# Optimization experiments

Measured on AMD Instinct MI355X. Metric: run time of the kernel, lower is better.

The kernel has to match this reference:

```python
import jax, jax.numpy as jnp
import numpy as np


def setup_inputs() -> dict:
    key = jax.random.key(0)
    k1, k2, k3, k4 = jax.random.split(key, 4)
    B, C_in, KH, KW, C_out = 256, 512, 7, 7, 1000
    inputR = jax.random.normal(k1, (B, C_in, KH, KW), dtype=jnp.float32)
    inputSPD = jax.random.normal(k2, (B, C_in, C_in), dtype=jnp.float32)
    fan_in = C_in * KH * KW
    weight = jax.random.normal(k3, (C_out, C_in, KH, KW), dtype=jnp.float32) / np.sqrt(fan_in)
    bias = jax.random.normal(k4, (C_out,), dtype=jnp.float32) / np.sqrt(fan_in)
    return {"inputR": inputR, "inputSPD": inputSPD, "weight": weight, "bias": bias}


def reference(inputR, inputSPD, weight, bias):
    # Conv2d with kernel == spatial size and padding 0 == fully connected layer.
    # outputR: (N, C_out)
    outputR = jnp.einsum('nchw,ochw->no', inputR, weight) + bias

    # top-2 channel selection per sample (indices only; values unused)
    _, top2_idx = jax.lax.top_k(outputR, 2)  # (N, 2)

    # weight is detached for the SPD path in the original module
    w_spd = jax.lax.stop_gradient(weight)[top2_idx]  # (N, 2, C_in, KH, KW)

    # outputSPD[n,k,m] = sum_{c,d,h,w} SPD[n,c,d] * W2[n,k,d,h,w] * W2[n,m,c,h,w]
    # (equivalent to the original's two batched matmuls + sum over (h, w))
    outputSPD = jnp.einsum('ncd,nkdhw,nmchw->nkm', inputSPD, w_spd, w_spd)  # (N, 2, 2)
    return outputR, outputSPD
```

## Files before the change

kernel.cpp:

```cpp
#include <hip/hip_runtime.h>

#define KD 25088
#define N_DIM 1000
#define ZS 28

typedef __attribute__((ext_vector_type(8))) short bf16x8;
typedef __attribute__((ext_vector_type(4))) float f32x4;

__device__ inline unsigned pack2(float a, float b) {
  unsigned r;
  asm("v_cvt_pk_bf16_f32 %0, %1, %2" : "=v"(r) : "v"(a), "v"(b));
  return r;
}
__device__ inline unsigned short f2bf(float x) {
  unsigned r;
  asm("v_cvt_pk_bf16_f32 %0, %1, %1" : "=v"(r) : "v"(x));
  return (unsigned short)r;
}
__device__ inline float bf2f(unsigned short u) {
  union { unsigned u; float f; } v; v.u = ((unsigned)u) << 16; return v.f;
}

__global__ __launch_bounds__(256) void init_bias_k(
    const float* __restrict__ bias, float* __restrict__ outR) {
  const int id = blockIdx.x * 256 + threadIdx.x;
  if (id < 256 * N_DIM) outR[id] = bias[id % N_DIM];
}

template<int ATOMIC>
__global__ __launch_bounds__(256) void rgemm_k(
    const float* __restrict__ A, const float* __restrict__ W,
    float* __restrict__ D) {
  __shared__ unsigned short As[2][128 * 32];
  __shared__ unsigned short Bs[2][128 * 32];
  const int t = threadIdx.x;
  const int id  = blockIdx.x;
  const int mz  = (id & 7) * 7 + ((id >> 3) >> 3);
  const int n0  = ((id >> 3) & 7) * 128;
  const int m0  = (mz / ZS) * 128;
  const int z   = mz % ZS;
  const int lane = t & 63, w = t >> 6;
  const int cw = (w >> 1) * 64, jw = (w & 1) * 64;
  const int r16 = lane & 15, quad = lane >> 4;
  const int srow = t >> 2;
  const int sc8  = (t & 3) << 3;
  const bool doj3 = (n0 + jw + 48) < N_DIM;

  float a_pre[16], b_pre[16];

  f32x4 acc[4][4];
#pragma unroll
  for (int i = 0; i < 4; ++i)
#pragma unroll
    for (int j = 0; j < 4; ++j) {
      acc[i][j][0] = 0.f; acc[i][j][1] = 0.f;
      acc[i][j][2] = 0.f; acc[i][j][3] = 0.f;
    }

#define RG_LOAD(s_)                                                         \
  {                                                                         \
    const int kbase = ((z) * ZS + (s_)) * 32;                               \
    _Pragma("unroll")                                                       \
    for (int h = 0; h < 2; ++h) {                                           \
      const int row = h * 64 + srow;                                        \
      const float* pa = A + (size_t)(m0 + row) * KD + kbase + sc8;          \
      *(float4*)&a_pre[h * 8 + 0] = *(const float4*)pa;                     \
      *(float4*)&a_pre[h * 8 + 4] = *(const float4*)(pa + 4);               \
      const int wr = n0 + row;                                              \
      if (wr < N_DIM) {                                                     \
        const float* pw = W + (size_t)wr * KD + kbase + sc8;                \
        *(float4*)&b_pre[h * 8 + 0] = *(const float4*)pw;                   \
        *(float4*)&b_pre[h * 8 + 4] = *(const float4*)(pw + 4);             \
      } else {                                                              \
        _Pragma("unroll")                                                   \
        for (int q = 0; q < 8; ++q) b_pre[h * 8 + q] = 0.f;                 \
      }                                                                     \
    }                                                                       \
  }

#define RG_WRITE(p_)                                                        \
  {                                                                         \
    _Pragma("unroll")                                                       \
    for (int h = 0; h < 2; ++h) {                                           \
      const int row = h * 64 + srow;                                        \
      uint4 ua, ub;                                                         \
      ua.x = pack2(a_pre[h*8+0], a_pre[h*8+1]);                             \
      ua.y = pack2(a_pre[h*8+2], a_pre[h*8+3]);                             \
      ua.z = pack2(a_pre[h*8+4], a_pre[h*8+5]);                             \
      ua.w = pack2(a_pre[h*8+6], a_pre[h*8+7]);                             \
      ub.x = pack2(b_pre[h*8+0], b_pre[h*8+1]);                             \
      ub.y = pack2(b_pre[h*8+2], b_pre[h*8+3]);                             \
      ub.z = pack2(b_pre[h*8+4], b_pre[h*8+5]);                             \
      ub.w = pack2(b_pre[h*8+6], b_pre[h*8+7]);                             \
      *(uint4*)&As[p_][row * 32 + sc8] = ua;                                \
      *(uint4*)&Bs[p_][row * 32 + sc8] = ub;                                \
    }                                                                       \
  }

  RG_LOAD(0); RG_WRITE(0); __syncthreads();
  int p = 0;
  for (int s = 0; s < ZS; ++s) {
    if (s + 1 < ZS) RG_LOAD(s + 1);
    bf16x8 af[4], bq[4];
#pragma unroll
    for (int i = 0; i < 4; ++i) {
      af[i] = *(const bf16x8*)&As[p][(cw + i * 16 + r16) * 32 + quad * 8];
      if (i < 3 || doj3)
        bq[i] = *(const bf16x8*)&Bs[p][(jw + i * 16 + r16) * 32 + quad * 8];
    }
#pragma unroll
    for (int i = 0; i < 4; ++i)
#pragma unroll
      for (int j = 0; j < 4; ++j)
        if (j < 3 || doj3)
          acc[i][j] = __builtin_amdgcn_mfma_f32_16x16x32_bf16(af[i], bq[j], acc[i][j], 0, 0, 0);
    if (s + 1 < ZS) RG_WRITE(p ^ 1);
    __syncthreads();
    p ^= 1;
  }

#pragma unroll
  for (int j = 0; j < 4; ++j) {
    const int n = n0 + jw + j * 16 + r16;
    if (n < N_DIM) {
#pragma unroll
      for (int i = 0; i < 4; ++i)
#pragma unroll
        for (int r = 0; r < 4; ++r) {
          const int m = m0 + cw + i * 16 + quad * 4 + r;
          if (ATOMIC)
            atomicAdd(&D[(size_t)m * N_DIM + n], acc[i][j][r]);
          else
            D[((size_t)z * 256 + m) * N_DIM + n] = acc[i][j][r];
        }
    }
  }
#undef RG_LOAD
#undef RG_WRITE
}

template<int FROMPART>
__global__ __launch_bounds__(64) void top8_k(
    const float* __restrict__ src, const float* __restrict__ bias,
    float* __restrict__ outR, int* __restrict__ top2,
    int* __restrict__ candIdx, int* __restrict__ flags,
    float* __restrict__ outSPD) {
  const int n = blockIdx.x;
  const int lane = threadIdx.x;
  float v[16];
  if (FROMPART) {
#pragma unroll
    for (int r = 0; r < 16; ++r) {
      const int o = lane + r * 64;
      v[r] = (o < N_DIM) ? bias[o] : -3.0e38f;
    }
    for (int z = 0; z < ZS; ++z) {
      const float* pz = src + ((size_t)z * 256 + n) * N_DIM;
#pragma unroll
      for (int r = 0; r < 16; ++r) {
        const int o = lane + r * 64;
        if (o < N_DIM) v[r] += pz[o];
      }
    }
#pragma unroll
    for (int r = 0; r < 16; ++r) {
      const int o = lane + r * 64;
      if (o < N_DIM) outR[(size_t)n * N_DIM + o] = v[r];
    }
  } else {
#pragma unroll
    for (int r = 0; r < 16; ++r) {
      const int o = lane + r * 64;
      v[r] = (o < N_DIM) ? src[(size_t)n * N_DIM + o] : -3.0e38f;
    }
  }
  float cv[8]; int ci[8];
#pragma unroll
  for (int rr = 0; rr < 8; ++rr) {
    float bv = -3.0e38f; int bi = 0x3fffffff;
#pragma unroll
    for (int r = 0; r < 16; ++r) {
      const int o = lane + r * 64;
      if (v[r] > bv || (v[r] == bv && o < bi)) { bv = v[r]; bi = o; }
    }
#pragma unroll
    for (int off = 32; off >= 1; off >>= 1) {
      const float ov = __shfl_xor(bv, off, 64);
      const int   oi = __shfl_xor(bi, off, 64);
      if (ov > bv || (ov == bv && oi < bi)) { bv = ov; bi = oi; }
    }
    cv[rr] = bv; ci[rr] = bi;
#pragma unroll
    for (int r = 0; r < 16; ++r)
      if (lane + r * 64 == bi) v[r] = -3.0e38f;
  }
  if (lane == 0) {
    const bool safe = (cv[0] - cv[1] >= 0.025f) &&
                      (cv[1] - cv[2] >= 0.025f) &&
                      (cv[1] - cv[7] >= 0.05f);
    flags[n] = safe ? 0 : 1;
    top2[2 * n]     = ci[0];
    top2[2 * n + 1] = ci[1];
#pragma unroll
    for (int r = 0; r < 8; ++r) candIdx[n * 8 + r] = ci[r];
    outSPD[4 * n + 0] = 0.f; outSPD[4 * n + 1] = 0.f;
    outSPD[4 * n + 2] = 0.f; outSPD[4 * n + 3] = 0.f;
  }
}

__global__ __launch_bounds__(256) void rdot_k(
    const float* __restrict__ A, const float* __restrict__ W,
    const float* __restrict__ bias, const int* __restrict__ candIdx,
    const int* __restrict__ flags, float* __restrict__ vals) {
  const int n = blockIdx.x;
  if (!flags[n]) return;
  const int c = blockIdx.y;
  const int idx = candIdx[n * 8 + c];
  const float4* a4 = (const float4*)(A + (size_t)n * KD);
  const float4* w4 = (const float4*)(W + (size_t)idx * KD);
  float s = 0.f;
  for (int i = threadIdx.x; i < KD / 4; i += 256) {
    const float4 av = a4[i];
    const float4 wv = w4[i];
    s += av.x * wv.x + av.y * wv.y + av.z * wv.z + av.w * wv.w;
  }
#pragma unroll
  for (int off = 32; off >= 1; off >>= 1) s += __shfl_xor(s, off, 64);
  __shared__ float red[4];
  const int lane = threadIdx.x & 63, w = threadIdx.x >> 6;
  if (lane == 0) red[w] = s;
  __syncthreads();
  if (threadIdx.x == 0)
    vals[n * 8 + c] = red[0] + red[1] + red[2] + red[3] + bias[idx];
}

__global__ __launch_bounds__(64) void select_k(
    const float* __restrict__ vals, const int* __restrict__ candIdx,
    const int* __restrict__ flags, int* __restrict__ top2) {
  const int n = blockIdx.x;
  if (threadIdx.x != 0 || !flags[n]) return;
  int b0 = -1; float v0 = -3.0e38f; int i0 = 0x3fffffff;
  for (int c = 0; c < 8; ++c) {
    const int idx = candIdx[n * 8 + c];
    const float vv = vals[n * 8 + c];
    if (vv > v0 || (vv == v0 && idx < i0)) { v0 = vv; i0 = idx; b0 = c; }
  }
  float v1 = -3.0e38f; int i1 = 0x3fffffff;
  for (int c = 0; c < 8; ++c) {
    if (c == b0) continue;
    const int idx = candIdx[n * 8 + c];
    const float vv = vals[n * 8 + c];
    if (vv > v1 || (vv == v1 && idx < i1)) { v1 = vv; i1 = idx; }
  }
  top2[2 * n]     = i0;
  top2[2 * n + 1] = i1;
}

__global__ __launch_bounds__(256) void packsel_k(
    const float* __restrict__ W, const int* __restrict__ candIdx,
    const int* __restrict__ flags, const float* __restrict__ vals,
    unsigned short* __restrict__ Wp) {
  __shared__ unsigned short tile[49 * 130];
  __shared__ int sel_s;
  const int n = blockIdx.x;
  const int which = blockIdx.y;
  const int t = threadIdx.x;
  if (t == 0) {
    int ia, ib;
    if (!flags[n]) {
      ia = candIdx[n * 8];
      ib = candIdx[n * 8 + 1];
    } else {
      int b0 = -1; float v0 = -3.0e38f; int i0 = 0x3fffffff;
      for (int c = 0; c < 8; ++c) {
        const int idx = candIdx[n * 8 + c];
        const float vv = vals[n * 8 + c];
        if (vv > v0 || (vv == v0 && idx < i0)) { v0 = vv; i0 = idx; b0 = c; }
      }
      float v1 = -3.0e38f; int i1 = 0x3fffffff;
      for (int c = 0; c < 8; ++c) {
        if (c == b0) continue;
        const int idx = candIdx[n * 8 + c];
        const float vv = vals[n * 8 + c];
        if (vv > v1 || (vv == v1 && idx < i1)) { v1 = vv; i1 = idx; }
      }
      ia = i0; ib = i1;
    }
    sel_s = which ? ib : ia;
  }
  unsigned short* dstn = Wp + (size_t)n * 65536;
  {
    const int r0 = 98 + which * 15;
    for (int u = t; u < 15 * 128; u += 256) {
      const int rr = u >> 7;
      const int cc = (u & 127) << 1;
      *(unsigned*)(dstn + (size_t)(r0 + rr) * 512 + cc) = 0u;
    }
  }
  __syncthreads();
  const int sel = sel_s;
  const float4* src4 = (const float4*)(W + (size_t)sel * KD);
  for (int chunk = 0; chunk < 4; ++chunk) {
    const float4* s4 = src4 + chunk * 1568;
    for (int u4 = t; u4 < 1568; u4 += 256) {
      const float4 fv = s4[u4];
      const float vv[4] = {fv.x, fv.y, fv.z, fv.w};
      const int i0 = u4 * 4;
#pragma unroll
      for (int e = 0; e < 4; ++e) {
        const int idx = i0 + e;
        const int c = idx / 49;
        const int hw = idx - c * 49;
        tile[hw * 130 + c] = f2bf(vv[e]);
      }
    }
    __syncthreads();
    const int cp = t & 63, hwb = t >> 6;
    unsigned short* wbase = dstn + (size_t)which * 49 * 512 + chunk * 128 + 2 * cp;
#pragma unroll
    for (int it = 0; it < 13; ++it) {
      const int hw = hwb + it * 4;
      if (hw < 49) {
        const unsigned val = *(const unsigned*)&tile[hw * 130 + 2 * cp];
        *(unsigned*)(wbase + (size_t)hw * 512) = val;
      }
    }
    __syncthreads();
  }
}

__global__ __launch_bounds__(256) void spd_k(
    const float* __restrict__ S, const unsigned short* __restrict__ Wp,
    float* __restrict__ outSPD) {
  __shared__ unsigned short As[2][128 * 32];
  __shared__ unsigned short Bs[2][128 * 32];
  __shared__ float red[4];
  const int t = threadIdx.x;
  const int id = blockIdx.x;
  const int n  = (id & 7) * 32 + ((id >> 3) >> 2);
  const int c0 = ((id >> 3) & 3) * 128;
  const float* Sn = S + (size_t)n * 512 * 512;
  const unsigned short* Wpn = Wp + (size_t)n * 65536;
  const int lane = t & 63, w = t >> 6;
  const int cw = (w >> 1) * 64, jw = (w & 1) * 64;
  const int r16 = lane & 15, quad = lane >> 4;
  const int srow = t >> 2;
  const int sc8  = (t & 3) << 3;
  const bool doj3 = (jw == 0);

  if (t < 4) red[t] = 0.f;

  float a_pre[16];
  uint4 b_pre[2];

  f32x4 acc[4][4];
#pragma unroll
  for (int i = 0; i < 4; ++i)
#pragma unroll
    for (int j = 0; j < 4; ++j) {
      acc[i][j][0] = 0.f; acc[i][j][1] = 0.f;
      acc[i][j][2] = 0.f; acc[i][j][3] = 0.f;
    }

#define SP_LOAD(s_)                                                         \
  {                                                                         \
    const int d0 = (s_) * 32;                                               \
    _Pragma("unroll")                                                       \
    for (int h = 0; h < 2; ++h) {                                           \
      const int row = h * 64 + srow;                                        \
      const float* pa = Sn + (size_t)(c0 + row) * 512 + d0 + sc8;           \
      *(float4*)&a_pre[h * 8 + 0] = *(const float4*)pa;                     \
      *(float4*)&a_pre[h * 8 + 4] = *(const float4*)(pa + 4);               \
      b_pre[h] = *(const uint4*)(Wpn + (size_t)row * 512 + d0 + sc8);       \
    }                                                                       \
  }

#define SP_WRITE(p_)                                                        \
  {                                                                         \
    _Pragma("unroll")                                                       \
    for (int h = 0; h < 2; ++h) {                                           \
      const int row = h * 64 + srow;                                        \
      uint4 ua;                                                             \
      ua.x = pack2(a_pre[h*8+0], a_pre[h*8+1]);                             \
      ua.y = pack2(a_pre[h*8+2], a_pre[h*8+3]);                             \
      ua.z = pack2(a_pre[h*8+4], a_pre[h*8+5]);                             \
      ua.w = pack2(a_pre[h*8+6], a_pre[h*8+7]);                             \
      *(uint4*)&As[p_][row * 32 + sc8] = ua;                                \
      *(uint4*)&Bs[p_][row * 32 + sc8] = b_pre[h];                          \
    }                                                                       \
  }

  SP_LOAD(0); SP_WRITE(0); __syncthreads();
  int p = 0;
  for (int s = 0; s < 16; ++s) {
    if (s + 1 < 16) SP_LOAD(s + 1);
    bf16x8 af[4], bq[4];
#pragma unroll
    for (int i = 0; i < 4; ++i) {
      af[i] = *(const bf16x8*)&As[p][(cw + i * 16 + r16) * 32 + quad * 8];
      if (i < 3 || doj3)
        bq[i] = *(const bf16x8*)&Bs[p][(jw + i * 16 + r16) * 32 + quad * 8];
    }
#pragma unroll
    for (int i = 0; i < 4; ++i)
#pragma unroll
      for (int j = 0; j < 4; ++j)
        if (j < 3 || doj3)
          acc[i][j] = __builtin_amdgcn_mfma_f32_16x16x32_bf16(af[i], bq[j], acc[i][j], 0, 0, 0);
    if (s + 1 < 16) SP_WRITE(p ^ 1);
    __syncthreads();
    p ^= 1;
  }
#undef SP_LOAD
#undef SP_WRITE

  float p00 = 0.f, p01 = 0.f, p10 = 0.f, p11 = 0.f;
#pragma unroll
  for (int j = 0; j < 4; ++j) {
    const int jj = jw + j * 16 + r16;
    if (jj < 98) {
      const int kk = (jj >= 49);
      const int hw = jj - 49 * kk;
      const unsigned short* wa = Wpn + (size_t)hw * 512;
      const unsigned short* wb = Wpn + (size_t)(49 + hw) * 512;
#pragma unroll
      for (int i = 0; i < 4; ++i) {
#pragma unroll
        for (int r = 0; r < 4; ++r) {
          const int c = c0 + cw + i * 16 + quad * 4 + r;
          const float u   = acc[i][j][r];
          const float wav = bf2f(wa[c]);
          const float wbv = bf2f(wb[c]);
          if (kk == 0) { p00 = fmaf(u, wav, p00); p01 = fmaf(u, wbv, p01); }
          else         { p10 = fmaf(u, wav, p10); p11 = fmaf(u, wbv, p11); }
        }
      }
    }
  }

  atomicAdd(&red[0], p00);
  atomicAdd(&red[1], p01);
  atomicAdd(&red[2], p10);
  atomicAdd(&red[3], p11);
  __syncthreads();
  if (t < 4) atomicAdd(&outSPD[n * 4 + t], red[t]);
}

__global__ __launch_bounds__(256) void spd_fb_k(
    const float* __restrict__ S, const float* __restrict__ W,
    const int* __restrict__ top2, float* __restrict__ outSPD) {
  __shared__ unsigned short As[128 * 40];
  __shared__ unsigned short Bs[128 * 40];
  __shared__ float red[4];
  const int t = threadIdx.x;
  const int n  = blockIdx.x >> 2;
  const int c0 = (blockIdx.x & 3) * 128;
  const int ia = top2[2 * n];
  const int ib = top2[2 * n + 1];
  const float* Sn = S + (size_t)n * 512 * 512;
  const int lane = t & 63, w = t >> 6;
  const int cw = (w >> 1) * 64, jw = (w & 1) * 64;
  const int r16 = lane & 15, quad = lane >> 4;
  if (t < 4) red[t] = 0.f;
  f32x4 acc[4][4];
#pragma unroll
  for (int i = 0; i < 4; ++i)
#pragma unroll
    for (int j = 0; j < 4; ++j) {
      acc[i][j][0] = 0.f; acc[i][j][1] = 0.f;
      acc[i][j][2] = 0.f; acc[i][j][3] = 0.f;
    }
  const int bj  = t & 127;
  const int bh  = t >> 7;
  const int bkk = (bj >= 49);
  const int bhw = bj - 49 * bkk;
  const bool bvalid = (bj < 98);
  const float* brow = W + (size_t)(bkk ? ib : ia) * KD + bhw;
  for (int d0 = 0; d0 < 512; d0 += 32) {
#pragma unroll
    for (int h = 0; h < 4; ++h) {
      const int idx = h * 256 + t;
      const int row = idx >> 3;
      const int c4  = (idx & 7) << 2;
      float4 av = *(const float4*)(Sn + (size_t)(c0 + row) * 512 + d0 + c4);
      uint2 pa;
      pa.x = pack2(av.x, av.y);
      pa.y = pack2(av.z, av.w);
      *(uint2*)&As[row * 40 + c4] = pa;
    }
#pragma unroll
    for (int dd2 = 0; dd2 < 16; dd2 += 2) {
      const int dd = bh * 16 + dd2;
      const float x0 = bvalid ? brow[(size_t)(d0 + dd) * 49] : 0.f;
      const float x1 = bvalid ? brow[(size_t)(d0 + dd + 1) * 49] : 0.f;
      *(unsigned*)&Bs[bj * 40 + dd] = pack2(x0, x1);
    }
    __syncthreads();
    bf16x8 af[4], bq[4];
#pragma unroll
    for (int i = 0; i < 4; ++i) {
      af[i] = *(const bf16x8*)&As[(cw + i * 16 + r16) * 40 + quad * 8];
      bq[i] = *(const bf16x8*)&Bs[(jw + i * 16 + r16) * 40 + quad * 8];
    }
#pragma unroll
    for (int i = 0; i < 4; ++i)
#pragma unroll
      for (int j = 0; j < 4; ++j)
        acc[i][j] = __builtin_amdgcn_mfma_f32_16x16x32_bf16(af[i], bq[j], acc[i][j], 0, 0, 0);
    __syncthreads();
  }
  float p00 = 0.f, p01 = 0.f, p10 = 0.f, p11 = 0.f;
  const float* Wa = W + (size_t)ia * KD;
  const float* Wb = W + (size_t)ib * KD;
#pragma unroll
  for (int j = 0; j < 4; ++j) {
    const int jj = jw + j * 16 + r16;
    if (jj < 98) {
      const int kk = (jj >= 49);
      const int hw = jj - 49 * kk;
#pragma unroll
      for (int i = 0; i < 4; ++i)
#pragma unroll
        for (int r = 0; r < 4; ++r) {
          const int c = c0 + cw + i * 16 + quad * 4 + r;
          const float u  = acc[i][j][r];
          const float wa = Wa[(size_t)c * 49 + hw];
          const float wb = Wb[(size_t)c * 49 + hw];
          if (kk == 0) { p00 = fmaf(u, wa, p00); p01 = fmaf(u, wb, p01); }
          else         { p10 = fmaf(u, wa, p10); p11 = fmaf(u, wb, p11); }
        }
    }
  }
  atomicAdd(&red[0], p00);
  atomicAdd(&red[1], p01);
  atomicAdd(&red[2], p10);
  atomicAdd(&red[3], p11);
  __syncthreads();
  if (t < 4) atomicAdd(&outSPD[n * 4 + t], red[t]);
}

extern "C" void kernel_launch(void* const* d_in, const int* in_sizes, int n_in,
                              void* d_out, int out_size, void* d_ws, size_t ws_size,
                              hipStream_t stream) {
  const float* inputR   = (const float*)d_in[0];
  const float* inputSPD = (const float*)d_in[1];
  const float* weight   = (const float*)d_in[2];
  const float* bias     = (const float*)d_in[3];
  float* out = (float*)d_out;

  int*   top2    = (int*)d_ws;
  int*   candIdx = (int*)((char*)d_ws + 2048);
  int*   flags   = (int*)((char*)d_ws + 2048 + 8192);
  float* vals    = (float*)((char*)d_ws + 2048 + 8192 + 1024);
  float* part    = (float*)((char*)d_ws + 65536);
  const size_t PART_BYTES = (size_t)ZS * 256 * N_DIM * 4;
  unsigned short* Wp = (unsigned short*)((char*)d_ws + 65536 + PART_BYTES);
  const bool bigws = ws_size >= 65536ull + PART_BYTES + 256ull * 65536ull * 2ull;

  if (bigws) {
    rgemm_k<0><<<dim3(448), 256, 0, stream>>>(inputR, weight, part);
    top8_k<1><<<dim3(256), 64, 0, stream>>>(part, bias, out, top2, candIdx, flags, out + 256000);
    rdot_k<<<dim3(256, 8), 256, 0, stream>>>(inputR, weight, bias, candIdx, flags, vals);
    packsel_k<<<dim3(256, 2), 256, 0, stream>>>(weight, candIdx, flags, vals, Wp);
    spd_k<<<dim3(1024), 256, 0, stream>>>(inputSPD, Wp, out + 256000);
  } else {
    init_bias_k<<<dim3(1000), 256, 0, stream>>>(bias, out);
    rgemm_k<1><<<dim3(448), 256, 0, stream>>>(inputR, weight, out);
    top8_k<0><<<dim3(256), 64, 0, stream>>>(out, bias, out, top2, candIdx, flags, out + 256000);
    rdot_k<<<dim3(256, 8), 256, 0, stream>>>(inputR, weight, bias, candIdx, flags, vals);
    select_k<<<dim3(256), 64, 0, stream>>>(vals, candIdx, flags, top2);
    spd_fb_k<<<dim3(1024), 256, 0, stream>>>(inputSPD, weight, top2, out + 256000);
  }
}
```

Baseline: 627.5 us.

## Load MFMA fragments directly from global memory, dropping LDS staging in GEMMs

Both the output GEMM and the SPD GEMM stop staging tiles through double-buffered shared memory. Each lane now loads and converts its own MFMA fragments straight from global memory, which removes the LDS writes, reads and per-step barriers. In exchange, each tile row is fetched by both wave pairs that share it, doubling global/L2 traffic. The software prefetch of the next k-step is also gone, so memory latency is exposed unless occupancy hides it.

```diff
diff --git a/kernel.cpp b/kernel.cpp
--- a/kernel.cpp
+++ b/kernel.cpp
@@ -21,6 +21,17 @@
   union { unsigned u; float f; } v; v.u = ((unsigned)u) << 16; return v.f;
 }
 
+__device__ inline bf16x8 ld_cvt8(const float* __restrict__ p) {
+  union { bf16x8 v; unsigned u[4]; } r;
+  const float4 a = *(const float4*)p;
+  const float4 b = *(const float4*)(p + 4);
+  r.u[0] = pack2(a.x, a.y);
+  r.u[1] = pack2(a.z, a.w);
+  r.u[2] = pack2(b.x, b.y);
+  r.u[3] = pack2(b.z, b.w);
+  return r.v;
+}
+
 __global__ __launch_bounds__(256) void init_bias_k(
     const float* __restrict__ bias, float* __restrict__ outR) {
   const int id = blockIdx.x * 256 + threadIdx.x;
@@ -31,8 +42,6 @@
 __global__ __launch_bounds__(256) void rgemm_k(
     const float* __restrict__ A, const float* __restrict__ W,
     float* __restrict__ D) {
-  __shared__ unsigned short As[2][128 * 32];
-  __shared__ unsigned short Bs[2][128 * 32];
   const int t = threadIdx.x;
   const int id  = blockIdx.x;
   const int mz  = (id & 7) * 7 + ((id >> 3) >> 3);
@@ -42,11 +51,7 @@
   const int lane = t & 63, w = t >> 6;
   const int cw = (w >> 1) * 64, jw = (w & 1) * 64;
   const int r16 = lane & 15, quad = lane >> 4;
-  const int srow = t >> 2;
-  const int sc8  = (t & 3) << 3;
   const bool doj3 = (n0 + jw + 48) < N_DIM;
-
-  float a_pre[16], b_pre[16];
 
   f32x4 acc[4][4];
 #pragma unroll
@@ -57,56 +62,29 @@
       acc[i][j][2] = 0.f; acc[i][j][3] = 0.f;
     }
 
-#define RG_LOAD(s_)                                                         \
-  {                                                                         \
-    const int kbase = ((z) * ZS + (s_)) * 32;                               \
-    _Pragma("unroll")                                                       \
-    for (int h = 0; h < 2; ++h) {                                           \
-      const int row = h * 64 + srow;                                        \
-      const float* pa = A + (size_t)(m0 + row) * KD + kbase + sc8;          \
-      *(float4*)&a_pre[h * 8 + 0] = *(const float4*)pa;                     \
-      *(float4*)&a_pre[h * 8 + 4] = *(const float4*)(pa + 4);               \
-      const int wr = n0 + row;                                              \
-      if (wr < N_DIM) {                                                     \
-        const float* pw = W + (size_t)wr * KD + kbase + sc8;                \
-        *(float4*)&b_pre[h * 8 + 0] = *(const float4*)pw;                   \
-        *(float4*)&b_pre[h * 8 + 4] = *(const float4*)(pw + 4);             \
-      } else {                                                              \
-        _Pragma("unroll")                                                   \
-        for (int q = 0; q < 8; ++q) b_pre[h * 8 + q] = 0.f;                 \
-      }                                                                     \
-    }                                                                       \
-  }
-
-#define RG_WRITE(p_)                                                        \
-  {                                                                         \
-    _Pragma("unroll")                                                       \
-    for (int h = 0; h < 2; ++h) {                                           \
-      const int row = h * 64 + srow;                                        \
-      uint4 ua, ub;                                                         \
-      ua.x = pack2(a_pre[h*8+0], a_pre[h*8+1]);                             \
-      ua.y = pack2(a_pre[h*8+2], a_pre[h*8+3]);                             \
-      ua.z = pack2(a_pre[h*8+4], a_pre[h*8+5]);                             \
-      ua.w = pack2(a_pre[h*8+6], a_pre[h*8+7]);                             \
-      ub.x = pack2(b_pre[h*8+0], b_pre[h*8+1]);                             \
-      ub.y = pack2(b_pre[h*8+2], b_pre[h*8+3]);                             \
-      ub.z = pack2(b_pre[h*8+4], b_pre[h*8+5]);                             \
-      ub.w = pack2(b_pre[h*8+6], b_pre[h*8+7]);                             \
-      *(uint4*)&As[p_][row * 32 + sc8] = ua;                                \
-      *(uint4*)&Bs[p_][row * 32 + sc8] = ub;                                \
-    }                                                                       \
-  }
-
-  RG_LOAD(0); RG_WRITE(0); __syncthreads();
-  int p = 0;
+  const float* arow[4];
+  const float* wrow[4];
+  bool wok[4];
+#pragma unroll
+  for (int i = 0; i < 4; ++i)
+    arow[i] = A + (size_t)(m0 + cw + i * 16 + r16) * KD + (size_t)z * (ZS * 32) + quad * 8;
+#pragma unroll
+  for (int j = 0; j < 4; ++j) {
+    const int n = n0 + jw + j * 16 + r16;
+    wok[j] = (n < N_DIM);
+    wrow[j] = W + (size_t)(wok[j] ? n : 0) * KD + (size_t)z * (ZS * 32) + quad * 8;
+  }
+
+  const bf16x8 zer = {0, 0, 0, 0, 0, 0, 0, 0};
   for (int s = 0; s < ZS; ++s) {
-    if (s + 1 < ZS) RG_LOAD(s + 1);
+    const int k0 = s * 32;
     bf16x8 af[4], bq[4];
 #pragma unroll
-    for (int i = 0; i < 4; ++i) {
-      af[i] = *(const bf16x8*)&As[p][(cw + i * 16 + r16) * 32 + quad * 8];
-      if (i < 3 || doj3)
-        bq[i] = *(const bf16x8*)&Bs[p][(jw + i * 16 + r16) * 32 + quad * 8];
+    for (int i = 0; i < 4; ++i) af[i] = ld_cvt8(arow[i] + k0);
+#pragma unroll
+    for (int j = 0; j < 4; ++j) {
+      if (j == 3 && !doj3) { bq[j] = zer; continue; }
+      bq[j] = wok[j] ? ld_cvt8(wrow[j] + k0) : zer;
     }
 #pragma unroll
     for (int i = 0; i < 4; ++i)
@@ -114,9 +92,6 @@
       for (int j = 0; j < 4; ++j)
         if (j < 3 || doj3)
           acc[i][j] = __builtin_amdgcn_mfma_f32_16x16x32_bf16(af[i], bq[j], acc[i][j], 0, 0, 0);
-    if (s + 1 < ZS) RG_WRITE(p ^ 1);
-    __syncthreads();
-    p ^= 1;
   }
 
 #pragma unroll
@@ -135,8 +110,6 @@
         }
     }
   }
-#undef RG_LOAD
-#undef RG_WRITE
 }
 
 template<int FROMPART>
@@ -332,8 +305,6 @@
 __global__ __launch_bounds__(256) void spd_k(
     const float* __restrict__ S, const unsigned short* __restrict__ Wp,
     float* __restrict__ outSPD) {
-  __shared__ unsigned short As[2][128 * 32];
-  __shared__ unsigned short Bs[2][128 * 32];
   __shared__ float red[4];
   const int t = threadIdx.x;
   const int id = blockIdx.x;
@@ -344,14 +315,9 @@
   const int lane = t & 63, w = t >> 6;
   const int cw = (w >> 1) * 64, jw = (w & 1) * 64;
   const int r16 = lane & 15, quad = lane >> 4;
-  const int srow = t >> 2;
-  const int sc8  = (t & 3) << 3;
   const bool doj3 = (jw == 0);
 
   if (t < 4) red[t] = 0.f;
-
-  float a_pre[16];
-  uint4 b_pre[2];
 
   f32x4 acc[4][4];
 #pragma unroll
@@ -362,57 +328,28 @@
       acc[i][j][2] = 0.f; acc[i][j][3] = 0.f;
     }
 
-#define SP_LOAD(s_)                                                         \
-  {                                                                         \
-    const int d0 = (s_) * 32;                                               \
-    _Pragma("unroll")                                                       \
-    for (int h = 0; h < 2; ++h) {                                           \
-      const int row = h * 64 + srow;                                        \
-      const float* pa = Sn + (size_t)(c0 + row) * 512 + d0 + sc8;           \
-      *(float4*)&a_pre[h * 8 + 0] = *(const float4*)pa;                     \
-      *(float4*)&a_pre[h * 8 + 4] = *(const float4*)(pa + 4);               \
-      b_pre[h] = *(const uint4*)(Wpn + (size_t)row * 512 + d0 + sc8);       \
-    }                                                                       \
-  }
-
-#define SP_WRITE(p_)                                                        \
-  {                                                                         \
-    _Pragma("unroll")                                                       \
-    for (int h = 0; h < 2; ++h) {                                           \
-      const int row = h * 64 + srow;                                        \
-      uint4 ua;                                                             \
-      ua.x = pack2(a_pre[h*8+0], a_pre[h*8+1]);                             \
-      ua.y = pack2(a_pre[h*8+2], a_pre[h*8+3]);                             \
-      ua.z = pack2(a_pre[h*8+4], a_pre[h*8+5]);                             \
-      ua.w = pack2(a_pre[h*8+6], a_pre[h*8+7]);                             \
-      *(uint4*)&As[p_][row * 32 + sc8] = ua;                                \
-      *(uint4*)&Bs[p_][row * 32 + sc8] = b_pre[h];                          \
-    }                                                                       \
-  }
-
-  SP_LOAD(0); SP_WRITE(0); __syncthreads();
-  int p = 0;
+  const float* sbase = Sn + (size_t)(c0 + cw + r16) * 512 + quad * 8;
+  const unsigned short* wbase = Wpn + (size_t)(jw + r16) * 512 + quad * 8;
+
   for (int s = 0; s < 16; ++s) {
-    if (s + 1 < 16) SP_LOAD(s + 1);
+    const int k0 = s * 32;
     bf16x8 af[4], bq[4];
 #pragma unroll
-    for (int i = 0; i < 4; ++i) {
-      af[i] = *(const bf16x8*)&As[p][(cw + i * 16 + r16) * 32 + quad * 8];
-      if (i < 3 || doj3)
-        bq[i] = *(const bf16x8*)&Bs[p][(jw + i * 16 + r16) * 32 + quad * 8];
-    }
+    for (int i = 0; i < 4; ++i)
+      af[i] = ld_cvt8(sbase + (size_t)i * 16 * 512 + k0);
+#pragma unroll
+    for (int j = 0; j < 4; ++j)
+      if (j < 3 || doj3)
+        bq[j] = *(const bf16x8*)(wbase + (size_t)j * 16 * 512 + k0);
 #pragma unroll
     for (int i = 0; i < 4; ++i)
 #pragma unroll
       for (int j = 0; j < 4; ++j)
         if (j < 3 || doj3)
           acc[i][j] = __builtin_amdgcn_mfma_f32_16x16x32_bf16(af[i], bq[j], acc[i][j], 0, 0, 0);
-    if (s + 1 < 16) SP_WRITE(p ^ 1);
-    __syncthreads();
-    p ^= 1;
-  }
-#undef SP_LOAD
-#undef SP_WRITE
+  }
+
+  __syncthreads();
 
   float p00 = 0.f, p01 = 0.f, p10 = 0.f, p11 = 0.f;
 #pragma unroll
```

Result: slower. 789.8 us (+25.9%).

## Split partial-sum reduction into wide kernel and read SPD weights directly

Applied to the files above, without the earlier changes.

Moves the summation of the 28 split-K partial results plus bias out of the 64-thread-per-sample top8 kernel into a separate 250-block kernel that reduces with float4 loads. The intent is to spread that memory-bound reduction across many more threads instead of 256 small blocks. Separately, the SPD GEMM stops staging the packed bf16 weight operand through shared memory and loads its MFMA fragments straight from global memory. That cuts LDS traffic and frees shared memory, but the fragment loads are no longer coalesced through a shared tile. It also adds one extra kernel launch and a write and re-read of outR.

```diff
diff --git a/kernel.cpp b/kernel.cpp
--- a/kernel.cpp
+++ b/kernel.cpp
@@ -25,6 +25,21 @@
     const float* __restrict__ bias, float* __restrict__ outR) {
   const int id = blockIdx.x * 256 + threadIdx.x;
   if (id < 256 * N_DIM) outR[id] = bias[id % N_DIM];
+}
+
+__global__ __launch_bounds__(256) void reduce_k(
+    const float* __restrict__ part, const float* __restrict__ bias,
+    float* __restrict__ outR) {
+  const int t4 = blockIdx.x * 256 + threadIdx.x;
+  const int e0 = t4 * 4;
+  const int n0 = e0 % N_DIM;
+  float4 acc = *(const float4*)(bias + n0);
+#pragma unroll
+  for (int z = 0; z < ZS; ++z) {
+    const float4 pv = *(const float4*)(part + (size_t)z * 256 * N_DIM + e0);
+    acc.x += pv.x; acc.y += pv.y; acc.z += pv.z; acc.w += pv.w;
+  }
+  *(float4*)(outR + e0) = acc;
 }
 
 template<int ATOMIC>
@@ -139,40 +154,17 @@
 #undef RG_WRITE
 }
 
-template<int FROMPART>
 __global__ __launch_bounds__(64) void top8_k(
-    const float* __restrict__ src, const float* __restrict__ bias,
-    float* __restrict__ outR, int* __restrict__ top2,
+    const float* __restrict__ outR, int* __restrict__ top2,
     int* __restrict__ candIdx, int* __restrict__ flags,
     float* __restrict__ outSPD) {
   const int n = blockIdx.x;
   const int lane = threadIdx.x;
   float v[16];
-  if (FROMPART) {
-#pragma unroll
-    for (int r = 0; r < 16; ++r) {
-      const int o = lane + r * 64;
-      v[r] = (o < N_DIM) ? bias[o] : -3.0e38f;
-    }
-    for (int z = 0; z < ZS; ++z) {
-      const float* pz = src + ((size_t)z * 256 + n) * N_DIM;
-#pragma unroll
-      for (int r = 0; r < 16; ++r) {
-        const int o = lane + r * 64;
-        if (o < N_DIM) v[r] += pz[o];
-      }
-    }
-#pragma unroll
-    for (int r = 0; r < 16; ++r) {
-      const int o = lane + r * 64;
-      if (o < N_DIM) outR[(size_t)n * N_DIM + o] = v[r];
-    }
-  } else {
-#pragma unroll
-    for (int r = 0; r < 16; ++r) {
-      const int o = lane + r * 64;
-      v[r] = (o < N_DIM) ? src[(size_t)n * N_DIM + o] : -3.0e38f;
-    }
+#pragma unroll
+  for (int r = 0; r < 16; ++r) {
+    const int o = lane + r * 64;
+    v[r] = (o < N_DIM) ? outR[(size_t)n * N_DIM + o] : -3.0e38f;
   }
   float cv[8]; int ci[8];
 #pragma unroll
@@ -333,7 +325,6 @@
     const float* __restrict__ S, const unsigned short* __restrict__ Wp,
     float* __restrict__ outSPD) {
   __shared__ unsigned short As[2][128 * 32];
-  __shared__ unsigned short Bs[2][128 * 32];
   __shared__ float red[4];
   const int t = threadIdx.x;
   const int id = blockIdx.x;
@@ -351,7 +342,6 @@
   if (t < 4) red[t] = 0.f;
 
   float a_pre[16];
-  uint4 b_pre[2];
 
   f32x4 acc[4][4];
 #pragma unroll
@@ -361,6 +351,11 @@
       acc[i][j][0] = 0.f; acc[i][j][1] = 0.f;
       acc[i][j][2] = 0.f; acc[i][j][3] = 0.f;
     }
+
+  const unsigned short* wjb[4];
+#pragma unroll
+  for (int j = 0; j < 4; ++j)
+    wjb[j] = Wpn + (size_t)(jw + j * 16 + r16) * 512 + quad * 8;
 
 #define SP_LOAD(s_)                                                         \
   {                                                                         \
@@ -371,7 +366,6 @@
       const float* pa = Sn + (size_t)(c0 + row) * 512 + d0 + sc8;           \
       *(float4*)&a_pre[h * 8 + 0] = *(const float4*)pa;                     \
       *(float4*)&a_pre[h * 8 + 4] = *(const float4*)(pa + 4);               \
-      b_pre[h] = *(const uint4*)(Wpn + (size_t)row * 512 + d0 + sc8);       \
     }                                                                       \
   }
 
@@ -386,7 +380,6 @@
       ua.z = pack2(a_pre[h*8+4], a_pre[h*8+5]);                             \
       ua.w = pack2(a_pre[h*8+6], a_pre[h*8+7]);                             \
       *(uint4*)&As[p_][row * 32 + sc8] = ua;                                \
-      *(uint4*)&Bs[p_][row * 32 + sc8] = b_pre[h];                          \
     }                                                                       \
   }
 
@@ -394,12 +387,13 @@
   int p = 0;
   for (int s = 0; s < 16; ++s) {
     if (s + 1 < 16) SP_LOAD(s + 1);
+    const int k0 = s * 32;
     bf16x8 af[4], bq[4];
 #pragma unroll
     for (int i = 0; i < 4; ++i) {
       af[i] = *(const bf16x8*)&As[p][(cw + i * 16 + r16) * 32 + quad * 8];
       if (i < 3 || doj3)
-        bq[i] = *(const bf16x8*)&Bs[p][(jw + i * 16 + r16) * 32 + quad * 8];
+        bq[i] = *(const bf16x8*)(wjb[i] + k0);
     }
 #pragma unroll
     for (int i = 0; i < 4; ++i)
@@ -559,14 +553,15 @@
 
   if (bigws) {
     rgemm_k<0><<<dim3(448), 256, 0, stream>>>(inputR, weight, part);
-    top8_k<1><<<dim3(256), 64, 0, stream>>>(part, bias, out, top2, candIdx, flags, out + 256000);
+    reduce_k<<<dim3(250), 256, 0, stream>>>(part, bias, out);
+    top8_k<<<dim3(256), 64, 0, stream>>>(out, top2, candIdx, flags, out + 256000);
     rdot_k<<<dim3(256, 8), 256, 0, stream>>>(inputR, weight, bias, candIdx, flags, vals);
     packsel_k<<<dim3(256, 2), 256, 0, stream>>>(weight, candIdx, flags, vals, Wp);
     spd_k<<<dim3(1024), 256, 0, stream>>>(inputSPD, Wp, out + 256000);
   } else {
     init_bias_k<<<dim3(1000), 256, 0, stream>>>(bias, out);
     rgemm_k<1><<<dim3(448), 256, 0, stream>>>(inputR, weight, out);
-    top8_k<0><<<dim3(256), 64, 0, stream>>>(out, bias, out, top2, candIdx, flags, out + 256000);
+    top8_k<<<dim3(256), 64, 0, stream>>>(out, top2, candIdx, flags, out + 256000);
     rdot_k<<<dim3(256, 8), 256, 0, stream>>>(inputR, weight, bias, candIdx, flags, vals);
     select_k<<<dim3(256), 64, 0, stream>>>(vals, candIdx, flags, top2);
     spd_fb_k<<<dim3(1024), 256, 0, stream>>>(inputSPD, weight, top2, out + 256000);
```

After: 532.2 us. 15.2% less time.
